# Kernel tuning notes

Hardware: AMD Instinct MI355X
Metric: run time of the kernel (lower is better)

## Reference

```python
import jax, jax.numpy as jnp
import numpy as np

N_SRC_USERS = 120000
N_TGT_USERS = 100000
N_SHARED = 4096
N_USERS = N_SRC_USERS + N_TGT_USERS - N_SHARED  # 215904
N_SRC_ITEMS = 60000
N_TGT_ITEMS = 50000
N_S = N_USERS + N_SRC_ITEMS  # 275904 source graph nodes
N_T = N_USERS + N_TGT_ITEMS  # 265904 target graph nodes
D = 64
N_LAYERS = 3
T = 5.0
NNZ = 2000000


def _l2n(x):
    # F.normalize(p=2, dim=1) with eps=1e-12
    return x / jnp.maximum(jnp.linalg.norm(x, axis=1, keepdims=True), 1e-12)


def _spmm(idx, vals, x, n):
    # torch.sparse.mm(A, x) with A in COO form: gather cols, scale, scatter-add rows
    return jax.ops.segment_sum(vals[:, None] * x[idx[1]], idx[0], num_segments=n)


def _inter(src_all, tgt_all, mapping):
    # cross-domain transfer on the shared-user block
    su, si = src_all[:N_USERS], src_all[N_USERS:]
    tu, ti = tgt_all[:N_USERS], tgt_all[N_USERS:]
    src = su[:N_SHARED]
    tgt = tu[:N_SHARED]
    src_raw, tgt_raw = src, tgt
    s = jnp.exp((src @ mapping) @ tgt.T / T)  # [n_shared, n_shared], positive
    sr = s / jnp.maximum(jnp.sum(s, axis=1, keepdims=True), 1e-12)  # L1 row-normalize
    sc = s / jnp.maximum(jnp.sum(s, axis=0, keepdims=True), 1e-12)  # L1 col-normalize
    src = src + sr @ tgt
    tgt = tgt + sc.T @ src  # uses updated src, as in the torch code
    eye = jnp.eye(N_SHARED, dtype=s.dtype)
    adj_s = s @ s.T + eye
    adj_s = adj_s / jnp.sum(adj_s, axis=1, keepdims=True)  # D^-1 (A+I)
    adj_t = s.T @ s + eye
    adj_t = adj_t / jnp.sum(adj_t, axis=1, keepdims=True)
    for _ in range(3):
        src = _l2n(jax.nn.relu(adj_s @ src))
        tgt = _l2n(jax.nn.relu(adj_t @ tgt))
    src = (src_raw + src) * 0.5
    tgt = (tgt_raw + tgt) * 0.5
    su = su.at[:N_SHARED].set(src)
    tu = tu.at[:N_SHARED].set(tgt)
    return jnp.concatenate([su, si], 0), jnp.concatenate([tu, ti], 0)


def setup_inputs() -> dict:
    key = jax.random.key(0)
    ks = jax.random.split(key, 9)
    scale = 0.02  # small init so exp(logits/t) stays bounded, like xavier
    return {
        "src_user_emb": jax.random.normal(ks[0], (N_USERS, D), jnp.float32) * scale,
        "tgt_user_emb": jax.random.normal(ks[1], (N_USERS, D), jnp.float32) * scale,
        "src_item_emb": jax.random.normal(ks[2], (N_SRC_ITEMS, D), jnp.float32) * scale,
        "tgt_item_emb": jax.random.normal(ks[3], (N_TGT_ITEMS, D), jnp.float32) * scale,
        "mapping": jax.random.normal(ks[4], (D, D), jnp.float32) * scale,
        "adj_s_vals": jax.random.uniform(ks[5], (NNZ,), jnp.float32) * 0.05,
        "adj_t_vals": jax.random.uniform(ks[6], (NNZ,), jnp.float32) * 0.05,
        "adj_s_idx": jax.random.randint(ks[7], (2, NNZ), 0, N_S, jnp.int32),
        "adj_t_idx": jax.random.randint(ks[8], (2, NNZ), 0, N_T, jnp.int32),
    }


def reference(src_user_emb, tgt_user_emb, src_item_emb, tgt_item_emb, mapping,
              adj_s_vals, adj_t_vals, adj_s_idx, adj_t_idx):
    emb_s = jnp.concatenate([src_user_emb, src_item_emb], 0)  # [N_S, D]
    emb_t = jnp.concatenate([tgt_user_emb, tgt_item_emb], 0)  # [N_T, D]
    list_s = [emb_s]
    list_t = [emb_t]
    for k in range(N_LAYERS):
        emb_s = _spmm(adj_s_idx, adj_s_vals, emb_s, N_S)
        emb_t = _spmm(adj_t_idx, adj_t_vals, emb_t, N_T)
        if k == 0:  # deterministic stand-in for random.random() < 0.3
            emb_s, emb_t = _inter(emb_s, emb_t, mapping)
        list_s.append(_l2n(emb_s))
        list_t.append(_l2n(emb_t))
    all_s = jnp.concatenate(list_s, axis=1)  # [N_S, D*(n_layers+1)]
    all_t = jnp.concatenate(list_t, axis=1)  # [N_T, D*(n_layers+1)]
    # concat source||target node embeddings into a single output block
    return jnp.concatenate([all_s, all_t], axis=0)  # [N_S+N_T, 256]
```

## Files before the change

### kernel.cpp

```cpp
#include <hip/hip_runtime.h>
#include <cstdint>
#include <cstddef>

typedef __attribute__((ext_vector_type(8))) short short8;
typedef __attribute__((ext_vector_type(8))) unsigned short ushort8;
typedef __attribute__((ext_vector_type(4))) float f32x4;

#define D64 64
static constexpr int kNU   = 215904;
static constexpr int kNS   = 275904;
static constexpr int kNT   = 265904;
static constexpr int kNSH  = 4096;
static constexpr int kNNZ  = 2000000;
static constexpr float kTinv = 0.2f;
static constexpr int kBinCh = 8192;
static constexpr int kNBkS = (kNS + 511) / 512;
static constexpr int kNBkT = (kNT + 511) / 512;
static constexpr int kBktCap = 6144;

__device__ __forceinline__ unsigned short f2bf(float x) {
  unsigned u = __builtin_bit_cast(unsigned, x);
  u += 0x7FFFu + ((u >> 16) & 1u);
  return (unsigned short)(u >> 16);
}
__device__ __forceinline__ float bf2f(unsigned short h) {
  return __builtin_bit_cast(float, (unsigned)h << 16);
}
__device__ __forceinline__ void ntst4(float* p, float4 v) {
  f32x4 vv = __builtin_bit_cast(f32x4, v);
  __builtin_nontemporal_store(vv, reinterpret_cast<f32x4*>(p));
}

__global__ void init_misc(int* __restrict__ bCnt, float* __restrict__ rs, float* __restrict__ cs) {
  int i = blockIdx.x * 256 + threadIdx.x;
  if (i < 2048) bCnt[i] = 0;
  if (i < kNSH) { rs[i] = 0.f; cs[i] = 0.f; }
}

__global__ void bhisto(const int* __restrict__ s_idx, const int* __restrict__ t_idx,
                       int* __restrict__ bCnt) {
  const int* idx = blockIdx.y ? t_idx : s_idx;
  int* bc = bCnt + blockIdx.y * 1024;
  __shared__ int cnt[544];
  int t = threadIdx.x;
  int e0 = blockIdx.x * kBinCh;
  int ecnt = min(kBinCh, kNNZ - e0);
  for (int b = t; b < 544; b += 256) cnt[b] = 0;
  __syncthreads();
  for (int k = t; k < ecnt; k += 256) atomicAdd(&cnt[idx[e0 + k] >> 9], 1);
  __syncthreads();
  for (int b = t; b < 544; b += 256) {
    int c = cnt[b];
    if (c) atomicAdd(&bc[b], c);
  }
}

__global__ void bscan(const int* __restrict__ bCnt, int* __restrict__ bBase,
                      int* __restrict__ bCur) {
  int g = blockIdx.y;
  int nbk = g ? kNBkT : kNBkS;
  const int* in = bCnt + g * 1024;
  int* ob = bBase + g * 1056;
  int* oc = bCur + g * 1024;
  __shared__ int ts[256];
  int t = threadIdx.x;
  int local[4];
  int s = 0;
#pragma unroll
  for (int i = 0; i < 4; ++i) {
    int gi = t * 4 + i;
    int v = (gi < nbk) ? in[gi] : 0;
    local[i] = s;
    s += v;
  }
  ts[t] = s;
  __syncthreads();
  for (int off = 1; off < 256; off <<= 1) {
    int v = (t >= off) ? ts[t - off] : 0;
    __syncthreads();
    ts[t] += v;
    __syncthreads();
  }
  int excl = (t == 0) ? 0 : ts[t - 1];
#pragma unroll
  for (int i = 0; i < 4; ++i) {
    int gi = t * 4 + i;
    if (gi < nbk) { ob[gi] = excl + local[i]; oc[gi] = excl + local[i]; }
  }
  if (t == 255) ob[nbk] = kNNZ;
}

__global__ void bin_lds(const int* __restrict__ s_idx, const float* __restrict__ s_vals,
                        const int* __restrict__ t_idx, const float* __restrict__ t_vals,
                        int* __restrict__ bCur,
                        int2* __restrict__ sCV, int* __restrict__ sR,
                        int2* __restrict__ tCV, int* __restrict__ tR) {
  const int* idx = blockIdx.y ? t_idx : s_idx;
  const float* vals = blockIdx.y ? t_vals : s_vals;
  int2* CV = blockIdx.y ? tCV : sCV;
  int* R = blockIdx.y ? tR : sR;
  int* bc = bCur + blockIdx.y * 1024;
  __shared__ int rows[kBinCh];
  __shared__ int cnt[544];
  int t = threadIdx.x;
  int e0 = blockIdx.x * kBinCh;
  int ecnt = min(kBinCh, kNNZ - e0);
  for (int b = t; b < 544; b += 256) cnt[b] = 0;
  __syncthreads();
  for (int k = t; k < ecnt; k += 256) {
    int r = idx[e0 + k];
    rows[k] = r;
    atomicAdd(&cnt[r >> 9], 1);
  }
  __syncthreads();
  for (int b = t; b < 544; b += 256) {
    int c = cnt[b];
    if (c) cnt[b] = atomicAdd(&bc[b], c);
  }
  __syncthreads();
  for (int k = t; k < ecnt; k += 256) {
    int r = rows[k];
    int p = atomicAdd(&cnt[r >> 9], 1);
    CV[p] = make_int2(idx[kNNZ + e0 + k], __float_as_int(vals[e0 + k]));
    R[p] = r;
  }
}

__global__ void bucket_csr(const int2* __restrict__ sCV, const int* __restrict__ sR,
                           int* __restrict__ sPtr, int* __restrict__ sEnd, int2* __restrict__ sEV,
                           const int2* __restrict__ tCV, const int* __restrict__ tR,
                           int* __restrict__ tPtr, int* __restrict__ tEnd, int2* __restrict__ tEV,
                           const int* __restrict__ bBase) {
  const int n = blockIdx.y ? kNT : kNS;
  int b = blockIdx.x;
  int rb0 = b << 9;
  if (rb0 >= n) return;
  const int2* CV = blockIdx.y ? tCV : sCV;
  const int* R = blockIdx.y ? tR : sR;
  int* Ptr = blockIdx.y ? tPtr : sPtr;
  int* End = blockIdx.y ? tEnd : sEnd;
  int2* EV = blockIdx.y ? tEV : sEV;
  const int* bb = bBase + blockIdx.y * 1056;
  int base = bb[b];
  int endE = bb[b + 1];
  int cnt = endE - base;
  __shared__ int cs[512];
  __shared__ int ps[256];
  __shared__ int2 stage[kBktCap];
  int t = threadIdx.x;
  cs[t] = 0; cs[t + 256] = 0;
  __syncthreads();
  for (int i = base + t; i < endE; i += 256)
    atomicAdd(&cs[R[i] - rb0], 1);
  __syncthreads();
  int c0 = cs[2 * t], c1 = cs[2 * t + 1];
  ps[t] = c0 + c1;
  __syncthreads();
  for (int off = 1; off < 256; off <<= 1) {
    int v = (t >= off) ? ps[t - off] : 0;
    __syncthreads();
    ps[t] += v;
    __syncthreads();
  }
  int pb = (t == 0) ? 0 : ps[t - 1];
  {
    int g0 = rb0 + 2 * t, g1 = g0 + 1;
    if (g0 < n) { Ptr[g0] = base + pb;      End[g0] = base + pb + c0; }
    if (g1 < n) { Ptr[g1] = base + pb + c0; End[g1] = base + pb + c0 + c1; }
  }
  cs[2 * t] = pb;
  cs[2 * t + 1] = pb + c0;
  __syncthreads();
  for (int i = base + t; i < endE; i += 256) {
    int r = R[i] - rb0;
    int p = atomicAdd(&cs[r], 1);
    stage[p] = CV[i];
  }
  __syncthreads();
  for (int j = t; j < cnt; j += 256) EV[base + j] = stage[j];
}

__global__ void cvt_in(const float* __restrict__ su, const float* __restrict__ si,
                       const float* __restrict__ tu, const float* __restrict__ ti,
                       unsigned short* __restrict__ sub, unsigned short* __restrict__ tub,
                       float* __restrict__ out) {
  int g = blockIdx.x * 16 + (threadIdx.x >> 4);
  bool isS = g < kNS;
  int r = isS ? g : g - kNS;
  if (!isS && r >= kNT) return;
  const float* xu = isS ? su : tu;
  const float* xi = isS ? si : ti;
  int q = (threadIdx.x & 15) << 2;
  const float4 v = *reinterpret_cast<const float4*>(
      ((r < kNU) ? (xu + ((size_t)r << 6)) : (xi + ((size_t)(r - kNU) << 6))) + q);
  ntst4(out + (size_t)g * 256 + q, v);
  unsigned long long pk = (unsigned long long)f2bf(v.x) |
                          ((unsigned long long)f2bf(v.y) << 16) |
                          ((unsigned long long)f2bf(v.z) << 32) |
                          ((unsigned long long)f2bf(v.w) << 48);
  *reinterpret_cast<unsigned long long*>((isS ? sub : tub) + ((size_t)r << 6) + q) = pk;
}

__global__ void spmm1(const int* __restrict__ sPtr, const int* __restrict__ sEndA,
                      const int2* __restrict__ sEV,
                      const int* __restrict__ tPtr, const int* __restrict__ tEndA,
                      const int2* __restrict__ tEV,
                      const unsigned short* __restrict__ sub, const unsigned short* __restrict__ tub,
                      float* __restrict__ es1h, float* __restrict__ et1h,
                      unsigned short* __restrict__ es1b, unsigned short* __restrict__ et1b,
                      float* __restrict__ out) {
  int g = blockIdx.x * 32 + (threadIdx.x >> 3);
  bool isS = g < kNS;
  int r = isS ? g : g - kNS;
  if (!isS && r >= kNT) return;
  const int* Pp = isS ? sPtr : tPtr;
  const int* Pc = isS ? sEndA : tEndA;
  const int2* EV = isS ? sEV : tEV;
  const unsigned short* xb = isS ? sub : tub;
  int q = (threadIdx.x & 7) << 3;
  int beg = Pp[r], end = Pc[r];
  float acc[8] = {0.f, 0.f, 0.f, 0.f, 0.f, 0.f, 0.f, 0.f};
  int lim = end - 1;
  for (int i = beg; i < end; i += 8) {
    int2 ev[8];
#pragma unroll
    for (int k = 0; k < 8; ++k) ev[k] = EV[min(i + k, lim)];
    ushort8 xv[8];
#pragma unroll
    for (int k = 0; k < 8; ++k)
      xv[k] = *reinterpret_cast<const ushort8*>(xb + ((size_t)ev[k].x << 6) + q);
#pragma unroll
    for (int k = 0; k < 8; ++k) {
      float v = (i + k <= lim) ? __int_as_float(ev[k].y) : 0.f;
#pragma unroll
      for (int j = 0; j < 8; ++j)
        acc[j] = fmaf(v, bf2f((unsigned short)xv[k][j]), acc[j]);
    }
  }
  if (r < kNSH) {
    float* eh = isS ? es1h : et1h;
    *reinterpret_cast<float4*>(eh + ((size_t)r << 6) + q) =
        make_float4(acc[0], acc[1], acc[2], acc[3]);
    *reinterpret_cast<float4*>(eh + ((size_t)r << 6) + q + 4) =
        make_float4(acc[4], acc[5], acc[6], acc[7]);
  }
  {
    unsigned short* eb = isS ? es1b : et1b;
    ushort8 o;
#pragma unroll
    for (int j = 0; j < 8; ++j) o[j] = f2bf(acc[j]);
    *reinterpret_cast<ushort8*>(eb + ((size_t)r << 6) + q) = o;
  }
  float ss = 0.f;
#pragma unroll
  for (int j = 0; j < 8; ++j) ss += acc[j] * acc[j];
  ss += __shfl_xor(ss, 1); ss += __shfl_xor(ss, 2); ss += __shfl_xor(ss, 4);
  float inv = 1.f / fmaxf(sqrtf(ss), 1e-12f);
  if (r >= kNSH) {
    float* op = out + (size_t)g * 256 + 64 + q;
    ntst4(op, make_float4(acc[0] * inv, acc[1] * inv, acc[2] * inv, acc[3] * inv));
    ntst4(op + 4, make_float4(acc[4] * inv, acc[5] * inv, acc[6] * inv, acc[7] * inv));
  }
}

template <int WRITE_Y>
__global__ void spmm23(const int* __restrict__ sPtr, const int* __restrict__ sEndA,
                       const int2* __restrict__ sEV,
                       const int* __restrict__ tPtr, const int* __restrict__ tEndA,
                       const int2* __restrict__ tEV,
                       const unsigned short* __restrict__ xs, const unsigned short* __restrict__ xt,
                       unsigned short* __restrict__ ys, unsigned short* __restrict__ yt,
                       float* __restrict__ out, int coff) {
  int g = blockIdx.x * 32 + (threadIdx.x >> 3);
  bool isS = g < kNS;
  int r = isS ? g : g - kNS;
  if (!isS && r >= kNT) return;
  const int* Pp = isS ? sPtr : tPtr;
  const int* Pc = isS ? sEndA : tEndA;
  const int2* EV = isS ? sEV : tEV;
  const unsigned short* xb = isS ? xs : xt;
  int q = (threadIdx.x & 7) << 3;
  int beg = Pp[r], end = Pc[r];
  float acc[8] = {0.f, 0.f, 0.f, 0.f, 0.f, 0.f, 0.f, 0.f};
  int lim = end - 1;
  for (int i = beg; i < end; i += 8) {
    int2 ev[8];
#pragma unroll
    for (int k = 0; k < 8; ++k) ev[k] = EV[min(i + k, lim)];
    ushort8 xv[8];
#pragma unroll
    for (int k = 0; k < 8; ++k)
      xv[k] = *reinterpret_cast<const ushort8*>(xb + ((size_t)ev[k].x << 6) + q);
#pragma unroll
    for (int k = 0; k < 8; ++k) {
      float v = (i + k <= lim) ? __int_as_float(ev[k].y) : 0.f;
#pragma unroll
      for (int j = 0; j < 8; ++j)
        acc[j] = fmaf(v, bf2f((unsigned short)xv[k][j]), acc[j]);
    }
  }
  if (WRITE_Y) {
    unsigned short* yb = isS ? ys : yt;
    ushort8 o;
#pragma unroll
    for (int j = 0; j < 8; ++j) o[j] = f2bf(acc[j]);
    *reinterpret_cast<ushort8*>(yb + ((size_t)r << 6) + q) = o;
  }
  float ss = 0.f;
#pragma unroll
  for (int j = 0; j < 8; ++j) ss += acc[j] * acc[j];
  ss += __shfl_xor(ss, 1); ss += __shfl_xor(ss, 2); ss += __shfl_xor(ss, 4);
  float inv = 1.f / fmaxf(sqrtf(ss), 1e-12f);
  float* op = out + (size_t)g * 256 + coff + q;
  ntst4(op, make_float4(acc[0] * inv, acc[1] * inv, acc[2] * inv, acc[3] * inv));
  ntst4(op + 4, make_float4(acc[4] * inv, acc[5] * inv, acc[6] * inv, acc[7] * inv));
}

__global__ void prep_inter(const float* __restrict__ A, const float* __restrict__ M,
                           unsigned short* __restrict__ tmpbf,
                           const float* __restrict__ Tg, unsigned short* __restrict__ rowmaj,
                           unsigned short* __restrict__ colmaj) {
  int t = threadIdx.x;
  if (blockIdx.y == 0) {
    __shared__ float Xs[64][65];
    __shared__ float As[16][65];
    int r0 = blockIdx.x * 16;
    int d = t & 63, rg = t >> 6;
    float acc[4] = {0.f, 0.f, 0.f, 0.f};
    for (int l = t; l < 1024; l += 256) {
      int r = l >> 4, c = (l & 15) << 2;
      float4 xv = *reinterpret_cast<const float4*>(M + (size_t)r * D64 + c);
      Xs[r][c] = xv.x; Xs[r][c + 1] = xv.y; Xs[r][c + 2] = xv.z; Xs[r][c + 3] = xv.w;
    }
    {
      int r = t >> 4, c = (t & 15) << 2;
      float4 av = *reinterpret_cast<const float4*>(A + (size_t)(r0 + r) * D64 + c);
      As[r][c] = av.x; As[r][c + 1] = av.y; As[r][c + 2] = av.z; As[r][c + 3] = av.w;
    }
    __syncthreads();
    for (int k = 0; k < 64; ++k) {
      float xv = Xs[k][d];
#pragma unroll
      for (int rr = 0; rr < 4; ++rr) acc[rr] += As[rg * 4 + rr][k] * xv;
    }
#pragma unroll
    for (int rr = 0; rr < 4; ++rr)
      tmpbf[(size_t)(r0 + rg * 4 + rr) * D64 + d] = f2bf(acc[rr]);
  } else {
    if (blockIdx.x >= 64) return;
    __shared__ unsigned short tile[64][72];
    int r0 = blockIdx.x * 64;
    int r = t >> 2, cq = (t & 3) << 4;
    unsigned short buf[16] __attribute__((aligned(16)));
#pragma unroll
    for (int j = 0; j < 16; j += 4) {
      float4 v = *reinterpret_cast<const float4*>(Tg + (size_t)(r0 + r) * D64 + cq + j);
      buf[j] = f2bf(v.x); buf[j + 1] = f2bf(v.y); buf[j + 2] = f2bf(v.z); buf[j + 3] = f2bf(v.w);
    }
#pragma unroll
    for (int j = 0; j < 16; ++j) tile[r][cq + j] = buf[j];
    *reinterpret_cast<ushort8*>(&rowmaj[(size_t)(r0 + r) * D64 + cq]) =
        *reinterpret_cast<ushort8*>(&buf[0]);
    *reinterpret_cast<ushort8*>(&rowmaj[(size_t)(r0 + r) * D64 + cq + 8]) =
        *reinterpret_cast<ushort8*>(&buf[8]);
    __syncthreads();
    int c = t >> 2, rq = (t & 3) << 4;
#pragma unroll
    for (int j = 0; j < 16; ++j) buf[j] = tile[rq + j][c];
    *reinterpret_cast<ushort8*>(&colmaj[(size_t)c * kNSH + r0 + rq]) =
        *reinterpret_cast<ushort8*>(&buf[0]);
    *reinterpret_cast<ushort8*>(&colmaj[(size_t)c * kNSH + r0 + rq + 8]) =
        *reinterpret_cast<ushort8*>(&buf[8]);
  }
}

__global__ void expS_mfma(const unsigned short* __restrict__ Abf,
                          const unsigned short* __restrict__ Bbf,
                          unsigned short* __restrict__ Sbf, unsigned short* __restrict__ STbf,
                          float* __restrict__ rs, float* __restrict__ cs) {
  __shared__ unsigned short Cs[64][72];
  __shared__ float csred[4][64];
  int j0 = blockIdx.x * 64, i0 = blockIdx.y * 64;
  int t = threadIdx.x;
  int w = t >> 6, l = t & 63;
  int lr = l & 15, lk = (l >> 4) << 3;
  f32x4 acc[4] = {};
  const unsigned short* Ap = Abf + (size_t)(i0 + w * 16 + lr) * D64 + lk;
#pragma unroll
  for (int ks = 0; ks < 2; ++ks) {
    short8 a = *reinterpret_cast<const short8*>(Ap + ks * 32);
#pragma unroll
    for (int nt = 0; nt < 4; ++nt) {
      short8 b = *reinterpret_cast<const short8*>(
          Bbf + (size_t)(j0 + nt * 16 + lr) * D64 + ks * 32 + lk);
      acc[nt] = __builtin_amdgcn_mfma_f32_16x16x32_bf16(a, b, acc[nt], 0, 0, 0);
    }
  }
  float rowpart[4] = {0.f, 0.f, 0.f, 0.f};
#pragma unroll
  for (int nt = 0; nt < 4; ++nt) {
    float colpart = 0.f;
#pragma unroll
    for (int rg = 0; rg < 4; ++rg) {
      float e = __expf(acc[nt][rg] * kTinv);
      acc[nt][rg] = e;
      rowpart[rg] += e;
      colpart += e;
      Cs[w * 16 + (l >> 4) * 4 + rg][nt * 16 + lr] = f2bf(e);
    }
    float v = colpart;
    v += __shfl_xor(v, 16); v += __shfl_xor(v, 32);
    if (l < 16) csred[w][nt * 16 + l] = v;
  }
#pragma unroll
  for (int rg = 0; rg < 4; ++rg) {
    float v = rowpart[rg];
    v += __shfl_xor(v, 1); v += __shfl_xor(v, 2);
    v += __shfl_xor(v, 4); v += __shfl_xor(v, 8);
    if (lr == 0) atomicAdd(&rs[i0 + w * 16 + (l >> 4) * 4 + rg], v);
  }
  __syncthreads();
  if (t < 64) atomicAdd(&cs[j0 + t], csred[0][t] + csred[1][t] + csred[2][t] + csred[3][t]);
  {
    int r = t >> 2, cq = (t & 3) << 4;
    ushort8 v0 = *reinterpret_cast<const ushort8*>(&Cs[r][cq]);
    ushort8 v1 = *reinterpret_cast<const ushort8*>(&Cs[r][cq + 8]);
    *reinterpret_cast<ushort8*>(&Sbf[(size_t)(i0 + r) * kNSH + j0 + cq]) = v0;
    *reinterpret_cast<ushort8*>(&Sbf[(size_t)(i0 + r) * kNSH + j0 + cq + 8]) = v1;
    int c = t >> 2, rq = (t & 3) << 4;
    unsigned short buf[16] __attribute__((aligned(16)));
#pragma unroll
    for (int j = 0; j < 16; ++j) buf[j] = Cs[rq + j][c];
    *reinterpret_cast<ushort8*>(&STbf[(size_t)(j0 + c) * kNSH + i0 + rq]) =
        *reinterpret_cast<ushort8*>(&buf[0]);
    *reinterpret_cast<ushort8*>(&STbf[(size_t)(j0 + c) * kNSH + i0 + rq + 8]) =
        *reinterpret_cast<ushort8*>(&buf[8]);
  }
}

__global__ void rowred2(const unsigned short* __restrict__ Sbf, const float* __restrict__ cs,
                        float* __restrict__ Ds,
                        const unsigned short* __restrict__ STbf, const float* __restrict__ rs,
                        float* __restrict__ Dt) {
  const unsigned short* Sb = blockIdx.y ? STbf : Sbf;
  const float* w = blockIdx.y ? rs : cs;
  float* outp = blockIdx.y ? Dt : Ds;
  int i = blockIdx.x;
  const unsigned short* row = Sb + (size_t)i * kNSH;
  int t = threadIdx.x;
  float acc = 0.f;
  for (int j0 = t * 8; j0 < kNSH; j0 += 2048) {
    short8 v = *reinterpret_cast<const short8*>(row + j0);
#pragma unroll
    for (int j = 0; j < 8; ++j) acc += bf2f((unsigned short)v[j]) * w[j0 + j];
  }
#pragma unroll
  for (int o = 32; o; o >>= 1) acc += __shfl_xor(acc, o);
  __shared__ float red[4];
  if ((t & 63) == 0) red[t >> 6] = acc;
  __syncthreads();
  if (t == 0) outp[i] = red[0] + red[1] + red[2] + red[3] + 1.f;
}

__global__ void sgemm_bf(const unsigned short* __restrict__ aA, const unsigned short* __restrict__ xA,
                         float* __restrict__ pA,
                         const unsigned short* __restrict__ aB, const unsigned short* __restrict__ xB,
                         float* __restrict__ pB) {
  const unsigned short* A = (blockIdx.z == 0) ? aA : aB;
  const unsigned short* X = (blockIdx.z == 0) ? xA : xB;
  float* P = (blockIdx.z == 0) ? pA : pB;
  int t = threadIdx.x;
  int w = t >> 6, l = t & 63;
  int lr = l & 15, lk = (l >> 4) << 3;
  int m0 = blockIdx.x * 64 + w * 16;
  int k0 = blockIdx.y * 1024;
  f32x4 acc[4] = {};
  const unsigned short* Ap = A + (size_t)(m0 + lr) * kNSH + k0 + lk;
  const unsigned short* Xp = X + (size_t)lr * kNSH + k0 + lk;
  for (int ks = 0; ks < 32; ++ks) {
    short8 a = *reinterpret_cast<const short8*>(Ap + ks * 32);
#pragma unroll
    for (int nt = 0; nt < 4; ++nt) {
      short8 b = *reinterpret_cast<const short8*>(Xp + (size_t)nt * 16 * kNSH + ks * 32);
      acc[nt] = __builtin_amdgcn_mfma_f32_16x16x32_bf16(a, b, acc[nt], 0, 0, 0);
    }
  }
  float* Pp = P + ((size_t)blockIdx.y * kNSH + m0) * D64;
#pragma unroll
  for (int nt = 0; nt < 4; ++nt)
#pragma unroll
    for (int rg = 0; rg < 4; ++rg)
      Pp[(size_t)((l >> 4) * 4 + rg) * D64 + nt * 16 + lr] = acc[nt][rg];
}

template <int EPI>
__global__ void red_epi(const float* __restrict__ pA, const float* __restrict__ addA,
                        const float* __restrict__ scA, float* __restrict__ outA,
                        unsigned short* __restrict__ outTA, const float* __restrict__ rawA,
                        unsigned short* __restrict__ rmA,
                        const float* __restrict__ pB, const float* __restrict__ addB,
                        const float* __restrict__ scB, float* __restrict__ outB,
                        unsigned short* __restrict__ outTB, const float* __restrict__ rawB,
                        unsigned short* __restrict__ rmB,
                        float* __restrict__ gout) {
  const float* p = (blockIdx.y == 0) ? pA : pB;
  const float* add = (blockIdx.y == 0) ? addA : addB;
  const float* sc = (blockIdx.y == 0) ? scA : scB;
  float* out = (blockIdx.y == 0) ? outA : outB;
  unsigned short* outT = (blockIdx.y == 0) ? outTA : outTB;
  const float* raw = (blockIdx.y == 0) ? rawA : rawB;
  unsigned short* rm = (blockIdx.y == 0) ? rmA : rmB;
  __shared__ unsigned short tile[64][4];
  int t = threadIdx.x;
  int d = t & 63, rl = t >> 6;
  int r = blockIdx.x * 4 + rl;
  size_t off = (size_t)r * D64 + d;
  const size_t SL = (size_t)kNSH * D64;
  float s = p[off] + p[SL + off] + p[2 * SL + off] + p[3 * SL + off];
  float v;
  if (EPI == 0) {
    v = s;
  } else if (EPI == 1) {
    v = add[off] + s / fmaxf(sc[r], 1e-12f);
    out[off] = v;
  } else {
    float x = fmaxf((s + add[off]) / sc[r], 0.f);
    float ss = x * x;
#pragma unroll
    for (int o = 32; o; o >>= 1) ss += __shfl_xor(ss, o);
    v = x / fmaxf(sqrtf(ss), 1e-12f);
    if (EPI == 2) out[off] = v;
    else {
      float fv = 0.5f * (raw[off] + v);
      rm[off] = f2bf(fv);
      float s2 = fv * fv;
#pragma unroll
      for (int o = 32; o; o >>= 1) s2 += __shfl_xor(s2, o);
      float nv = fv / fmaxf(sqrtf(s2), 1e-12f);
      size_t grow0 = (blockIdx.y == 0) ? 0 : (size_t)kNS;
      __builtin_nontemporal_store(nv, &gout[(grow0 + (size_t)r) * 256 + 64 + d]);
    }
  }
  if (EPI != 3) {
    tile[d][rl] = f2bf(v);
    __syncthreads();
    if (t < 64) {
      unsigned long long pk;
      unsigned short* pp = reinterpret_cast<unsigned short*>(&pk);
      pp[0] = tile[t][0]; pp[1] = tile[t][1]; pp[2] = tile[t][2]; pp[3] = tile[t][3];
      *reinterpret_cast<unsigned long long*>(&outT[(size_t)t * kNSH + blockIdx.x * 4]) = pk;
    }
  }
}

extern "C" void kernel_launch(void* const* d_in, const int* in_sizes, int n_in,
                              void* d_out, int out_size, void* d_ws, size_t ws_size,
                              hipStream_t stream) {
  const float* src_user = (const float*)d_in[0];
  const float* tgt_user = (const float*)d_in[1];
  const float* src_item = (const float*)d_in[2];
  const float* tgt_item = (const float*)d_in[3];
  const float* mapping  = (const float*)d_in[4];
  const float* s_vals   = (const float*)d_in[5];
  const float* t_vals   = (const float*)d_in[6];
  const int*   s_idx    = (const int*)d_in[7];
  const int*   t_idx    = (const int*)d_in[8];
  float* out = (float*)d_out;

  float* w = (float*)d_ws;
  size_t o = 0;
  float* es1h = w + o; o += (size_t)kNSH * D64;
  float* et1h = w + o; o += (size_t)kNSH * D64;
  float* src2 = w + o; o += (size_t)kNSH * D64;
  float* tgt2 = w + o; o += (size_t)kNSH * D64;
  float* itS  = w + o; o += (size_t)kNSH * D64;
  float* itT  = w + o; o += (size_t)kNSH * D64;
  float* partA = w + o; o += (size_t)4 * kNSH * D64;
  float* partB = w + o; o += (size_t)4 * kNSH * D64;
  float* rs = w + o; o += kNSH;
  float* cs = w + o; o += kNSH;
  float* Ds = w + o; o += kNSH;
  float* Dt = w + o; o += kNSH;
  unsigned short* ub = (unsigned short*)(w + o);
  size_t uo = 0;
  unsigned short* Sbf   = ub + uo; uo += (size_t)kNSH * kNSH;
  unsigned short* STbf  = ub + uo; uo += (size_t)kNSH * kNSH;
  unsigned short* tmpbf = ub + uo; uo += (size_t)kNSH * D64;
  unsigned short* tgtbf = ub + uo; uo += (size_t)kNSH * D64;
  unsigned short* tgtT  = ub + uo; uo += (size_t)kNSH * D64;
  unsigned short* src2T = ub + uo; uo += (size_t)kNSH * D64;
  unsigned short* tgt2T = ub + uo; uo += (size_t)kNSH * D64;
  unsigned short* itST  = ub + uo; uo += (size_t)kNSH * D64;
  unsigned short* itTT  = ub + uo; uo += (size_t)kNSH * D64;
  unsigned short* ybAT  = ub + uo; uo += (size_t)kNSH * D64;
  unsigned short* ybBT  = ub + uo; uo += (size_t)kNSH * D64;
  unsigned short* sub   = ub + uo; uo += (size_t)kNS * D64;
  unsigned short* tub   = ub + uo; uo += (size_t)kNT * D64;
  unsigned short* es1b  = ub + uo; uo += (size_t)kNS * D64;
  unsigned short* et1b  = ub + uo; uo += (size_t)kNT * D64;
  unsigned short* es2b  = ub + uo; uo += (size_t)kNS * D64;
  unsigned short* et2b  = ub + uo; uo += (size_t)kNT * D64;
  int* iw = (int*)(ub + ((uo + 1) & ~(size_t)1));
  size_t io = 0;
  int* sPtr = iw + io; io += kNS;
  int* sEnd = iw + io; io += kNS;
  int* tPtr = iw + io; io += kNT;
  int* tEnd = iw + io; io += kNT;
  int* bCnt = iw + io; io += 2048;
  int* bCur = iw + io; io += 2048;
  int* bBase = iw + io; io += 2112;
  io = (io + 1) & ~(size_t)1;
  int2* sEV = (int2*)(iw + io); io += (size_t)2 * kNNZ;
  int2* tEV = (int2*)(iw + io); io += (size_t)2 * kNNZ;
  int2* sCV = (int2*)(iw + io); io += (size_t)2 * kNNZ;
  int2* tCV = (int2*)(iw + io); io += (size_t)2 * kNNZ;
  int* sR = iw + io; io += kNNZ;
  int* tR = iw + io; io += kNNZ;

  const int bgrid = (kNNZ + kBinCh - 1) / kBinCh;

  init_misc<<<16, 256, 0, stream>>>(bCnt, rs, cs);
  bhisto<<<dim3(bgrid, 2), 256, 0, stream>>>(s_idx, t_idx, bCnt);
  bscan<<<dim3(1, 2), 256, 0, stream>>>(bCnt, bBase, bCur);
  bin_lds<<<dim3(bgrid, 2), 256, 0, stream>>>(s_idx, s_vals, t_idx, t_vals, bCur,
                                              sCV, sR, tCV, tR);
  bucket_csr<<<dim3(kNBkS, 2), 256, 0, stream>>>(sCV, sR, sPtr, sEnd, sEV,
                                                 tCV, tR, tPtr, tEnd, tEV, bBase);

  cvt_in<<<(kNS + kNT + 15) / 16, 256, 0, stream>>>(src_user, src_item, tgt_user, tgt_item,
                                                    sub, tub, out);

  spmm1<<<(kNS + kNT + 31) / 32, 256, 0, stream>>>(sPtr, sEnd, sEV, tPtr, tEnd, tEV,
                                                   sub, tub, es1h, et1h, es1b, et1b, out);

  prep_inter<<<dim3(256, 2), 256, 0, stream>>>(es1h, mapping, tmpbf, et1h, tgtbf, tgtT);
  expS_mfma<<<dim3(64, 64), 256, 0, stream>>>(tmpbf, tgtbf, Sbf, STbf, rs, cs);
  rowred2<<<dim3(kNSH, 2), 256, 0, stream>>>(Sbf, cs, Ds, STbf, rs, Dt);
  sgemm_bf<<<dim3(64, 4, 1), 256, 0, stream>>>(Sbf, tgtT, partA, Sbf, tgtT, partA);
  red_epi<1><<<dim3(1024, 1), 256, 0, stream>>>(partA, es1h, rs, src2, src2T, nullptr, nullptr,
                                                partA, es1h, rs, src2, src2T, nullptr, nullptr, out);
  sgemm_bf<<<dim3(64, 4, 1), 256, 0, stream>>>(STbf, src2T, partA, STbf, src2T, partA);
  red_epi<1><<<dim3(1024, 1), 256, 0, stream>>>(partA, et1h, cs, tgt2, tgt2T, nullptr, nullptr,
                                                partA, et1h, cs, tgt2, tgt2T, nullptr, nullptr, out);
  float* paF = src2; unsigned short* paT = src2T;
  float* pbF = itS;  unsigned short* pbT = itST;
  float* qaF = tgt2; unsigned short* qaT = tgt2T;
  float* qbF = itT;  unsigned short* qbT = itTT;
  for (int itn = 0; itn < 3; ++itn) {
    sgemm_bf<<<dim3(64, 4, 2), 256, 0, stream>>>(STbf, paT, partA, Sbf, qaT, partB);
    red_epi<0><<<dim3(1024, 2), 256, 0, stream>>>(
        partA, nullptr, nullptr, nullptr, ybAT, nullptr, nullptr,
        partB, nullptr, nullptr, nullptr, ybBT, nullptr, nullptr, out);
    sgemm_bf<<<dim3(64, 4, 2), 256, 0, stream>>>(Sbf, ybAT, partA, STbf, ybBT, partB);
    if (itn < 2) {
      red_epi<2><<<dim3(1024, 2), 256, 0, stream>>>(
          partA, paF, Ds, pbF, pbT, nullptr, nullptr,
          partB, qaF, Dt, qbF, qbT, nullptr, nullptr, out);
      float* tf = paF; paF = pbF; pbF = tf;
      unsigned short* tt = paT; paT = pbT; pbT = tt;
      tf = qaF; qaF = qbF; qbF = tf;
      tt = qaT; qaT = qbT; qbT = tt;
    } else {
      red_epi<3><<<dim3(1024, 2), 256, 0, stream>>>(
          partA, paF, Ds, nullptr, nullptr, es1h, es1b,
          partB, qaF, Dt, nullptr, nullptr, et1h, et1b, out);
    }
  }

  spmm23<1><<<(kNS + kNT + 31) / 32, 256, 0, stream>>>(sPtr, sEnd, sEV, tPtr, tEnd, tEV,
                                                       es1b, et1b, es2b, et2b, out, 128);
  spmm23<0><<<(kNS + kNT + 31) / 32, 256, 0, stream>>>(sPtr, sEnd, sEV, tPtr, tEnd, tEV,
                                                       es2b, et2b, nullptr, nullptr, out, 192);
}
```

Before: 954.3 us.

## Drop histogram/scan passes by using fixed-stride row buckets with packed row offsets

```diff
diff --git a/kernel.cpp b/kernel.cpp
--- a/kernel.cpp
+++ b/kernel.cpp
@@ -16,7 +16,9 @@
 static constexpr int kBinCh = 8192;
 static constexpr int kNBkS = (kNS + 511) / 512;
 static constexpr int kNBkT = (kNT + 511) / 512;
+static constexpr int kBStride = 4608;
 static constexpr int kBktCap = 6144;
+static constexpr int kColMask = 0x7FFFF;
 
 __device__ __forceinline__ unsigned short f2bf(float x) {
   unsigned u = __builtin_bit_cast(unsigned, x);
@@ -31,74 +33,19 @@
   __builtin_nontemporal_store(vv, reinterpret_cast<f32x4*>(p));
 }
 
-__global__ void init_misc(int* __restrict__ bCnt, float* __restrict__ rs, float* __restrict__ cs) {
+__global__ void init_misc(int* __restrict__ bCur, float* __restrict__ rs, float* __restrict__ cs) {
   int i = blockIdx.x * 256 + threadIdx.x;
-  if (i < 2048) bCnt[i] = 0;
+  if (i < 2048) bCur[i] = (i & 1023) * kBStride;
   if (i < kNSH) { rs[i] = 0.f; cs[i] = 0.f; }
-}
-
-__global__ void bhisto(const int* __restrict__ s_idx, const int* __restrict__ t_idx,
-                       int* __restrict__ bCnt) {
-  const int* idx = blockIdx.y ? t_idx : s_idx;
-  int* bc = bCnt + blockIdx.y * 1024;
-  __shared__ int cnt[544];
-  int t = threadIdx.x;
-  int e0 = blockIdx.x * kBinCh;
-  int ecnt = min(kBinCh, kNNZ - e0);
-  for (int b = t; b < 544; b += 256) cnt[b] = 0;
-  __syncthreads();
-  for (int k = t; k < ecnt; k += 256) atomicAdd(&cnt[idx[e0 + k] >> 9], 1);
-  __syncthreads();
-  for (int b = t; b < 544; b += 256) {
-    int c = cnt[b];
-    if (c) atomicAdd(&bc[b], c);
-  }
-}
-
-__global__ void bscan(const int* __restrict__ bCnt, int* __restrict__ bBase,
-                      int* __restrict__ bCur) {
-  int g = blockIdx.y;
-  int nbk = g ? kNBkT : kNBkS;
-  const int* in = bCnt + g * 1024;
-  int* ob = bBase + g * 1056;
-  int* oc = bCur + g * 1024;
-  __shared__ int ts[256];
-  int t = threadIdx.x;
-  int local[4];
-  int s = 0;
-#pragma unroll
-  for (int i = 0; i < 4; ++i) {
-    int gi = t * 4 + i;
-    int v = (gi < nbk) ? in[gi] : 0;
-    local[i] = s;
-    s += v;
-  }
-  ts[t] = s;
-  __syncthreads();
-  for (int off = 1; off < 256; off <<= 1) {
-    int v = (t >= off) ? ts[t - off] : 0;
-    __syncthreads();
-    ts[t] += v;
-    __syncthreads();
-  }
-  int excl = (t == 0) ? 0 : ts[t - 1];
-#pragma unroll
-  for (int i = 0; i < 4; ++i) {
-    int gi = t * 4 + i;
-    if (gi < nbk) { ob[gi] = excl + local[i]; oc[gi] = excl + local[i]; }
-  }
-  if (t == 255) ob[nbk] = kNNZ;
 }
 
 __global__ void bin_lds(const int* __restrict__ s_idx, const float* __restrict__ s_vals,
                         const int* __restrict__ t_idx, const float* __restrict__ t_vals,
                         int* __restrict__ bCur,
-                        int2* __restrict__ sCV, int* __restrict__ sR,
-                        int2* __restrict__ tCV, int* __restrict__ tR) {
+                        int2* __restrict__ sCV, int2* __restrict__ tCV) {
   const int* idx = blockIdx.y ? t_idx : s_idx;
   const float* vals = blockIdx.y ? t_vals : s_vals;
   int2* CV = blockIdx.y ? tCV : sCV;
-  int* R = blockIdx.y ? tR : sR;
   int* bc = bCur + blockIdx.y * 1024;
   __shared__ int rows[kBinCh];
   __shared__ int cnt[544];
@@ -121,28 +68,26 @@
   for (int k = t; k < ecnt; k += 256) {
     int r = rows[k];
     int p = atomicAdd(&cnt[r >> 9], 1);
-    CV[p] = make_int2(idx[kNNZ + e0 + k], __float_as_int(vals[e0 + k]));
-    R[p] = r;
-  }
-}
-
-__global__ void bucket_csr(const int2* __restrict__ sCV, const int* __restrict__ sR,
+    CV[p] = make_int2(idx[kNNZ + e0 + k] | ((r & 511) << 19),
+                      __float_as_int(vals[e0 + k]));
+  }
+}
+
+__global__ void bucket_csr(const int2* __restrict__ sCV,
                            int* __restrict__ sPtr, int* __restrict__ sEnd, int2* __restrict__ sEV,
-                           const int2* __restrict__ tCV, const int* __restrict__ tR,
+                           const int2* __restrict__ tCV,
                            int* __restrict__ tPtr, int* __restrict__ tEnd, int2* __restrict__ tEV,
-                           const int* __restrict__ bBase) {
+                           const int* __restrict__ bCur) {
   const int n = blockIdx.y ? kNT : kNS;
   int b = blockIdx.x;
   int rb0 = b << 9;
   if (rb0 >= n) return;
   const int2* CV = blockIdx.y ? tCV : sCV;
-  const int* R = blockIdx.y ? tR : sR;
   int* Ptr = blockIdx.y ? tPtr : sPtr;
   int* End = blockIdx.y ? tEnd : sEnd;
   int2* EV = blockIdx.y ? tEV : sEV;
-  const int* bb = bBase + blockIdx.y * 1056;
-  int base = bb[b];
-  int endE = bb[b + 1];
+  int base = b * kBStride;
+  int endE = bCur[blockIdx.y * 1024 + b];
   int cnt = endE - base;
   __shared__ int cs[512];
   __shared__ int ps[256];
@@ -151,7 +96,7 @@
   cs[t] = 0; cs[t + 256] = 0;
   __syncthreads();
   for (int i = base + t; i < endE; i += 256)
-    atomicAdd(&cs[R[i] - rb0], 1);
+    atomicAdd(&cs[CV[i].x >> 19], 1);
   __syncthreads();
   int c0 = cs[2 * t], c1 = cs[2 * t + 1];
   ps[t] = c0 + c1;
@@ -172,9 +117,9 @@
   cs[2 * t + 1] = pb + c0;
   __syncthreads();
   for (int i = base + t; i < endE; i += 256) {
-    int r = R[i] - rb0;
-    int p = atomicAdd(&cs[r], 1);
-    stage[p] = CV[i];
+    int2 cv = CV[i];
+    int p = atomicAdd(&cs[cv.x >> 19], 1);
+    stage[p] = make_int2(cv.x & kColMask, cv.y);
   }
   __syncthreads();
   for (int j = t; j < cnt; j += 256) EV[base + j] = stage[j];
@@ -606,26 +551,20 @@
   int* sEnd = iw + io; io += kNS;
   int* tPtr = iw + io; io += kNT;
   int* tEnd = iw + io; io += kNT;
-  int* bCnt = iw + io; io += 2048;
   int* bCur = iw + io; io += 2048;
-  int* bBase = iw + io; io += 2112;
   io = (io + 1) & ~(size_t)1;
-  int2* sEV = (int2*)(iw + io); io += (size_t)2 * kNNZ;
-  int2* tEV = (int2*)(iw + io); io += (size_t)2 * kNNZ;
-  int2* sCV = (int2*)(iw + io); io += (size_t)2 * kNNZ;
-  int2* tCV = (int2*)(iw + io); io += (size_t)2 * kNNZ;
-  int* sR = iw + io; io += kNNZ;
-  int* tR = iw + io; io += kNNZ;
+  const size_t kPad = (size_t)544 * kBStride;
+  int2* sEV = (int2*)(iw + io); io += 2 * kPad;
+  int2* tEV = (int2*)(iw + io); io += 2 * kPad;
+  int2* sCV = (int2*)(iw + io); io += 2 * kPad;
+  int2* tCV = (int2*)(iw + io); io += 2 * kPad;
 
   const int bgrid = (kNNZ + kBinCh - 1) / kBinCh;
 
-  init_misc<<<16, 256, 0, stream>>>(bCnt, rs, cs);
-  bhisto<<<dim3(bgrid, 2), 256, 0, stream>>>(s_idx, t_idx, bCnt);
-  bscan<<<dim3(1, 2), 256, 0, stream>>>(bCnt, bBase, bCur);
-  bin_lds<<<dim3(bgrid, 2), 256, 0, stream>>>(s_idx, s_vals, t_idx, t_vals, bCur,
-                                              sCV, sR, tCV, tR);
-  bucket_csr<<<dim3(kNBkS, 2), 256, 0, stream>>>(sCV, sR, sPtr, sEnd, sEV,
-                                                 tCV, tR, tPtr, tEnd, tEV, bBase);
+  init_misc<<<16, 256, 0, stream>>>(bCur, rs, cs);
+  bin_lds<<<dim3(bgrid, 2), 256, 0, stream>>>(s_idx, s_vals, t_idx, t_vals, bCur, sCV, tCV);
+  bucket_csr<<<dim3(kNBkS, 2), 256, 0, stream>>>(sCV, sPtr, sEnd, sEV,
+                                                 tCV, tPtr, tEnd, tEV, bCur);
 
   cvt_in<<<(kNS + kNT + 15) / 16, 256, 0, stream>>>(src_user, src_item, tgt_user, tgt_item,
                                                     sub, tub, out);
```

Result: faster. 860.6 us (-9.8%).
